# Optimization experiments

Hardware: AMD Instinct MI355X
Metric: run time of the kernel (lower is better)

## Reference

```python
import jax, jax.numpy as jnp
import numpy as np


def setup_inputs() -> dict:
    key = jax.random.key(0)
    k1, k2, k3 = jax.random.split(key, 3)
    B, T, F, U = 32, 4096, 512, 512
    x = jax.random.normal(k1, (B, T, F), dtype=jnp.float32)
    W = jax.random.normal(k2, (F, U), dtype=jnp.float32)
    b = jnp.zeros((U,), dtype=jnp.float32)
    V = jax.random.uniform(k3, (U, 1), dtype=jnp.float32)
    return {"x": x, "W": W, "b": b, "V": V}


def reference(x, W, b, V):
    # u = tanh(x @ W + b): [B, T, U]
    u = jnp.tanh(jnp.einsum('btf,fu->btu', x, W) + b)
    # scores = u @ V: [B, T, 1]; softmax over time (dim=1)
    a = jax.nn.softmax(jnp.einsum('btu,uo->bto', u, V), axis=1)
    # weighted sum pooling over time -> [B, F]
    return jnp.sum(x * a, axis=1)
```

## Files before the change

### kernel.cpp

```cpp
#include <hip/hip_runtime.h>


#define XT 4096
#define XF 512
#define XU 512

typedef __attribute__((ext_vector_type(8))) short short8;
typedef __attribute__((ext_vector_type(4))) short sh4;
typedef __attribute__((ext_vector_type(16))) float f32x16;

__device__ inline void cvt_hilo(float x, unsigned short &h, unsigned short &l) {
  unsigned u = __builtin_bit_cast(unsigned, x);
  h = (unsigned short)(u >> 16);
  float hf = __builtin_bit_cast(float, u & 0xFFFF0000u);
  float lo = x - hf;
  l = (unsigned short)(__builtin_bit_cast(unsigned, lo) >> 16);
}

__device__ inline float tanh_fast(float z) {
  float e = __expf(2.0f * z);
  return 1.0f - 2.0f * __builtin_amdgcn_rcpf(e + 1.0f);
}

__global__ void wconv_kernel(const float *__restrict__ W,
                             unsigned short *__restrict__ whi,
                             unsigned short *__restrict__ wlo) {
  int t2 = blockIdx.x * 256 + threadIdx.x;
  int l = t2 & 31;
  int g = (t2 >> 5) & 1;
  int t = (t2 >> 6) & 15;
  int s = t2 >> 10;
  short8 hv, lv;
#pragma unroll
  for (int j = 0; j < 8; ++j) {
    unsigned short h, lo;
    cvt_hilo(W[(size_t)(s * 16 + g * 8 + j) * XU + t * 32 + l], h, lo);
    hv[j] = (short)h;
    lv[j] = (short)lo;
  }
  size_t off = (size_t)s * 8192 + t * 512 + g * 256 + l * 8;
  *(short8 *)(whi + off) = hv;
  *(short8 *)(wlo + off) = lv;
}

#define MFMA(a, b, c) __builtin_amdgcn_mfma_f32_32x32x16_bf16(a, b, c, 0, 0, 0)

__global__ __launch_bounds__(512, 4)
void gemm_scores_kernel(const float *__restrict__ x,
                        const unsigned short *__restrict__ whi,
                        const unsigned short *__restrict__ wlo,
                        const float *__restrict__ bias,
                        const float *__restrict__ V,
                        float *__restrict__ partial,
                        float *__restrict__ pstats) {
  __shared__ unsigned short Abuf[2][4096];
  __shared__ float scb[256];
  __shared__ float sarr[128];
  __shared__ float warr[128];
  __shared__ float red[1536];

  const int tid = threadIdx.x;
  const int lane = tid & 63;
  const int w = tid >> 6;
  const int l31 = lane & 31;
  const int half = lane >> 5;
  const size_t rowbase = (size_t)blockIdx.x * 128;

  const int srow = tid >> 4;
  const int q = tid & 15;
  const int widx = (q >> 2) * 1024 + ((q >> 1) & 1) * 256 + srow * 8 + (q & 1) * 4;

  auto stage = [&](unsigned short *ab, float4 v) {
    sh4 h, l;
    unsigned short hh, ll;
    cvt_hilo(v.x, hh, ll); h[0] = (short)hh; l[0] = (short)ll;
    cvt_hilo(v.y, hh, ll); h[1] = (short)hh; l[1] = (short)ll;
    cvt_hilo(v.z, hh, ll); h[2] = (short)hh; l[2] = (short)ll;
    cvt_hilo(v.w, hh, ll); h[3] = (short)hh; l[3] = (short)ll;
    *(sh4 *)(ab + widx) = h;
    *(sh4 *)(ab + widx + 512) = l;
  };

  const unsigned short *whp = whi + (size_t)(w * 2) * 512 + lane * 8;
  const unsigned short *wlp = wlo + (size_t)(w * 2) * 512 + lane * 8;

#pragma unroll 1
  for (int sub = 0; sub < 4; ++sub) {
    f32x16 acc[2];
#pragma unroll
    for (int c = 0; c < 2; ++c)
#pragma unroll
      for (int r = 0; r < 16; ++r) acc[c][r] = 0.f;

    const float *sx = x + (rowbase + sub * 32 + srow) * XF + q * 4;

    float4 xa = *(const float4 *)sx;
    stage(&Abuf[0][0], xa);
    __syncthreads();

#pragma unroll 1
    for (int it = 0; it < 8; ++it) {
      float4 xn;
      if (it < 7) xn = *(const float4 *)(sx + (it + 1) * 64);

      const unsigned short *abase = &Abuf[it & 1][0];
      const unsigned short *pw = whp + (size_t)it * 32768;
      const unsigned short *pl = wlp + (size_t)it * 32768;

#pragma unroll 2
      for (int s16 = 0; s16 < 4; ++s16) {
        short8 bh0 = *(const short8 *)(pw + s16 * 8192);
        short8 bh1 = *(const short8 *)(pw + s16 * 8192 + 512);
        short8 bl0 = *(const short8 *)(pl + s16 * 8192);
        short8 bl1 = *(const short8 *)(pl + s16 * 8192 + 512);
        short8 ah = *(const short8 *)(abase + s16 * 1024 + lane * 8);
        short8 al = *(const short8 *)(abase + s16 * 1024 + 512 + lane * 8);
        acc[0] = MFMA(ah, bh0, acc[0]);
        acc[1] = MFMA(ah, bh1, acc[1]);
        acc[0] = MFMA(al, bh0, acc[0]);
        acc[1] = MFMA(al, bh1, acc[1]);
        acc[0] = MFMA(ah, bl0, acc[0]);
        acc[1] = MFMA(ah, bl1, acc[1]);
      }

      if (it < 7) stage(&Abuf[(it + 1) & 1][0], xn);
      __syncthreads();
    }

    float sc[16];
#pragma unroll
    for (int r = 0; r < 16; ++r) sc[r] = 0.f;
#pragma unroll
    for (int cf = 0; cf < 2; ++cf) {
      int n = w * 64 + cf * 32 + l31;
      float vv = V[n];
      float bb = bias[n];
#pragma unroll
      for (int r = 0; r < 16; ++r)
        sc[r] += tanh_fast(acc[cf][r] + bb) * vv;
    }
#pragma unroll
    for (int m = 1; m <= 16; m <<= 1) {
#pragma unroll
      for (int r = 0; r < 16; ++r) sc[r] += __shfl_xor(sc[r], m, 64);
    }
    if (l31 == 0) {
#pragma unroll
      for (int r = 0; r < 16; ++r) {
        int row = (r & 3) + 8 * (r >> 2) + 4 * half;
        scb[w * 32 + row] = sc[r];
      }
    }
    __syncthreads();
    if (tid < 32) {
      float s = 0.f;
#pragma unroll
      for (int ww = 0; ww < 8; ++ww) s += scb[ww * 32 + tid];
      sarr[sub * 32 + tid] = s;
    }
    __syncthreads();
  }

  float mloc = -1e30f;
#pragma unroll 8
  for (int i = 0; i < 128; ++i) mloc = fmaxf(mloc, sarr[i]);
  if (tid < 128) warr[tid] = __expf(sarr[tid] - mloc);
  __syncthreads();

  float lsum = 0.f;
  if (tid < 64) {
    lsum = warr[tid] + warr[tid + 64];
#pragma unroll
    for (int m = 1; m < 64; m <<= 1) lsum += __shfl_xor(lsum, m, 64);
  }

  const int rg = tid >> 7;
  const int c4 = tid & 127;
  const float *xp = x + rowbase * XF;
  float4 pa = {0.f, 0.f, 0.f, 0.f};
#pragma unroll 8
  for (int i = 0; i < 32; ++i) {
    int r = rg * 32 + i;
    float4 v = *(const float4 *)(xp + (size_t)r * XF + c4 * 4);
    float wv = warr[r];
    pa.x += wv * v.x;
    pa.y += wv * v.y;
    pa.z += wv * v.z;
    pa.w += wv * v.w;
  }
  if (rg > 0) {
    float *rp = red + (rg - 1) * 512 + c4 * 4;
    rp[0] = pa.x; rp[1] = pa.y; rp[2] = pa.z; rp[3] = pa.w;
  }
  __syncthreads();
  if (rg == 0) {
    const float *r0 = red + c4 * 4;
    float4 o;
    o.x = pa.x + r0[0] + r0[512] + r0[1024];
    o.y = pa.y + r0[1] + r0[513] + r0[1025];
    o.z = pa.z + r0[2] + r0[514] + r0[1026];
    o.w = pa.w + r0[3] + r0[515] + r0[1027];
    *(float4 *)(partial + (size_t)blockIdx.x * 512 + c4 * 4) = o;
  }
  if (tid == 0) {
    pstats[blockIdx.x * 2] = mloc;
    pstats[blockIdx.x * 2 + 1] = lsum;
  }
}

__global__ __launch_bounds__(512)
void combine_kernel(const float *__restrict__ partial,
                    const float *__restrict__ pstats,
                    float *__restrict__ out) {
  int b = blockIdx.x;
  int f = threadIdx.x;
  __shared__ float ml[32], ll[32];
  if (f < 32) {
    ml[f] = pstats[(b * 32 + f) * 2];
    ll[f] = pstats[(b * 32 + f) * 2 + 1];
  }
  __syncthreads();
  float M = -1e30f;
#pragma unroll
  for (int c = 0; c < 32; ++c) M = fmaxf(M, ml[c]);
  float L = 0.f;
#pragma unroll
  for (int c = 0; c < 32; ++c) L += __expf(ml[c] - M) * ll[c];
  float acc = 0.f;
#pragma unroll
  for (int c = 0; c < 32; ++c)
    acc += __expf(ml[c] - M) * partial[(size_t)(b * 32 + c) * 512 + f];
  out[b * XF + f] = acc / L;
}

extern "C" void kernel_launch(void *const *d_in, const int *in_sizes, int n_in,
                              void *d_out, int out_size, void *d_ws,
                              size_t ws_size, hipStream_t stream) {
  const float *x = (const float *)d_in[0];
  const float *W = (const float *)d_in[1];
  const float *bias = (const float *)d_in[2];
  const float *V = (const float *)d_in[3];
  float *out = (float *)d_out;

  unsigned short *whi = (unsigned short *)d_ws;
  unsigned short *wlo = whi + 262144;
  float *partial = (float *)((char *)d_ws + 1048576);
  float *pstats = (float *)((char *)d_ws + 1048576 + 2097152);

  wconv_kernel<<<128, 256, 0, stream>>>(W, whi, wlo);
  gemm_scores_kernel<<<1024, 512, 0, stream>>>(x, whi, wlo, bias, V, partial,
                                               pstats);
  combine_kernel<<<32, 512, 0, stream>>>(partial, pstats, out);
}
```

Measured before the change: 565.6 us.

## Stage W tiles in shared memory and keep 128x256 accumulators per wave group

The GEMM loop is restructured. Each block now keeps all 128 rows resident across 8 waves, arranged as 4 row slices by 2 column halves with 8 accumulator tiles each. The split-bf16 W tiles are double-buffered through shared memory and the x fragments are converted straight from registers, instead of staging x in LDS and streaming W from global per wave. The goal is more MFMA work per loaded byte, better W reuse and fewer barriers. The cost is 128 KB of shared memory and higher register pressure, which forces the occupancy hint down from 4 to 2 blocks per CU.

```diff
diff --git a/kernel.cpp b/kernel.cpp
--- a/kernel.cpp
+++ b/kernel.cpp
@@ -6,7 +6,6 @@
 #define XU 512
 
 typedef __attribute__((ext_vector_type(8))) short short8;
-typedef __attribute__((ext_vector_type(4))) short sh4;
 typedef __attribute__((ext_vector_type(16))) float f32x16;
 
 __device__ inline void cvt_hilo(float x, unsigned short &h, unsigned short &l) {
@@ -45,7 +44,7 @@
 
 #define MFMA(a, b, c) __builtin_amdgcn_mfma_f32_32x32x16_bf16(a, b, c, 0, 0, 0)
 
-__global__ __launch_bounds__(512, 4)
+__global__ __launch_bounds__(512, 2)
 void gemm_scores_kernel(const float *__restrict__ x,
                         const unsigned short *__restrict__ whi,
                         const unsigned short *__restrict__ wlo,
@@ -53,7 +52,7 @@
                         const float *__restrict__ V,
                         float *__restrict__ partial,
                         float *__restrict__ pstats) {
-  __shared__ unsigned short Abuf[2][4096];
+  __shared__ unsigned short Bsh[2][4][8192];
   __shared__ float scb[256];
   __shared__ float sarr[128];
   __shared__ float warr[128];
@@ -61,106 +60,135 @@
 
   const int tid = threadIdx.x;
   const int lane = tid & 63;
-  const int w = tid >> 6;
+  const int wave = tid >> 6;
+  const int rs = wave & 3;
+  const int c = wave >> 2;
   const int l31 = lane & 31;
   const int half = lane >> 5;
   const size_t rowbase = (size_t)blockIdx.x * 128;
 
-  const int srow = tid >> 4;
-  const int q = tid & 15;
-  const int widx = (q >> 2) * 1024 + ((q >> 1) & 1) * 256 + srow * 8 + (q & 1) * 4;
-
-  auto stage = [&](unsigned short *ab, float4 v) {
-    sh4 h, l;
-    unsigned short hh, ll;
-    cvt_hilo(v.x, hh, ll); h[0] = (short)hh; l[0] = (short)ll;
-    cvt_hilo(v.y, hh, ll); h[1] = (short)hh; l[1] = (short)ll;
-    cvt_hilo(v.z, hh, ll); h[2] = (short)hh; l[2] = (short)ll;
-    cvt_hilo(v.w, hh, ll); h[3] = (short)hh; l[3] = (short)ll;
-    *(sh4 *)(ab + widx) = h;
-    *(sh4 *)(ab + widx + 512) = l;
-  };
-
-  const unsigned short *whp = whi + (size_t)(w * 2) * 512 + lane * 8;
-  const unsigned short *wlp = wlo + (size_t)(w * 2) * 512 + lane * 8;
+  f32x16 acc[8];
+#pragma unroll
+  for (int cf = 0; cf < 8; ++cf)
+#pragma unroll
+    for (int r = 0; r < 16; ++r) acc[cf][r] = 0.f;
+
+  const float *xr = x + (rowbase + rs * 32 + l31) * XF + half * 8;
+  const int toff = tid * 8;
+  const int fbase = (c * 8) * 512 + lane * 8;
+
+  short8 st0, st1, st2, st3, st4, st5, st6, st7;
+  float4 xa0, xa1, xa2, xa3;
+
+#define LOADSTG(J)                                                   \
+  {                                                                  \
+    const unsigned short *ph = whi + (size_t)(2 * (J)) * 8192;       \
+    const unsigned short *pl = wlo + (size_t)(2 * (J)) * 8192;       \
+    st0 = *(const short8 *)(ph + toff);                              \
+    st1 = *(const short8 *)(ph + 4096 + toff);                       \
+    st2 = *(const short8 *)(pl + toff);                              \
+    st3 = *(const short8 *)(pl + 4096 + toff);                       \
+    st4 = *(const short8 *)(ph + 8192 + toff);                       \
+    st5 = *(const short8 *)(ph + 12288 + toff);                      \
+    st6 = *(const short8 *)(pl + 8192 + toff);                       \
+    st7 = *(const short8 *)(pl + 12288 + toff);                      \
+  }
+#define WRITESTG(BUF)                                                \
+  {                                                                  \
+    unsigned short *d = &Bsh[BUF][0][0] + toff;                      \
+    *(short8 *)(d) = st0;                                            \
+    *(short8 *)(d + 4096) = st1;                                     \
+    *(short8 *)(d + 8192) = st2;                                     \
+    *(short8 *)(d + 12288) = st3;                                    \
+    *(short8 *)(d + 16384) = st4;                                    \
+    *(short8 *)(d + 20480) = st5;                                    \
+    *(short8 *)(d + 24576) = st6;                                    \
+    *(short8 *)(d + 28672) = st7;                                    \
+  }
+#define LOADA(J)                                                     \
+  {                                                                  \
+    xa0 = *(const float4 *)(xr + (J) * 32);                          \
+    xa1 = *(const float4 *)(xr + (J) * 32 + 4);                      \
+    xa2 = *(const float4 *)(xr + (J) * 32 + 16);                     \
+    xa3 = *(const float4 *)(xr + (J) * 32 + 20);                     \
+  }
+
+  LOADSTG(0);
+  LOADA(0);
+  WRITESTG(0);
+  __syncthreads();
 
 #pragma unroll 1
-  for (int sub = 0; sub < 4; ++sub) {
-    f32x16 acc[2];
-#pragma unroll
-    for (int c = 0; c < 2; ++c)
-#pragma unroll
-      for (int r = 0; r < 16; ++r) acc[c][r] = 0.f;
-
-    const float *sx = x + (rowbase + sub * 32 + srow) * XF + q * 4;
-
-    float4 xa = *(const float4 *)sx;
-    stage(&Abuf[0][0], xa);
+  for (int j = 0; j < 16; ++j) {
+    const int cur = j & 1;
+
+    short8 ah0, al0, ah1, al1;
+    {
+      float v0[8] = {xa0.x, xa0.y, xa0.z, xa0.w, xa1.x, xa1.y, xa1.z, xa1.w};
+      float v1[8] = {xa2.x, xa2.y, xa2.z, xa2.w, xa3.x, xa3.y, xa3.z, xa3.w};
+#pragma unroll
+      for (int jj = 0; jj < 8; ++jj) {
+        unsigned short h, lo;
+        cvt_hilo(v0[jj], h, lo);
+        ah0[jj] = (short)h; al0[jj] = (short)lo;
+        cvt_hilo(v1[jj], h, lo);
+        ah1[jj] = (short)h; al1[jj] = (short)lo;
+      }
+    }
+
+    if (j < 15) {
+      LOADSTG(j + 1);
+      LOADA(j + 1);
+    }
+
+#pragma unroll
+    for (int h = 0; h < 2; ++h) {
+      const unsigned short *bp = &Bsh[cur][h * 2][0] + fbase;
+      const unsigned short *lp = bp + 8192;
+      short8 ahf = h ? ah1 : ah0;
+      short8 alf = h ? al1 : al0;
+#pragma unroll
+      for (int cf = 0; cf < 8; ++cf) {
+        short8 bh = *(const short8 *)(bp + cf * 512);
+        short8 bl = *(const short8 *)(lp + cf * 512);
+        acc[cf] = MFMA(ahf, bh, acc[cf]);
+        acc[cf] = MFMA(alf, bh, acc[cf]);
+        acc[cf] = MFMA(ahf, bl, acc[cf]);
+      }
+    }
+
+    if (j < 15) WRITESTG(cur ^ 1);
     __syncthreads();
-
-#pragma unroll 1
-    for (int it = 0; it < 8; ++it) {
-      float4 xn;
-      if (it < 7) xn = *(const float4 *)(sx + (it + 1) * 64);
-
-      const unsigned short *abase = &Abuf[it & 1][0];
-      const unsigned short *pw = whp + (size_t)it * 32768;
-      const unsigned short *pl = wlp + (size_t)it * 32768;
-
-#pragma unroll 2
-      for (int s16 = 0; s16 < 4; ++s16) {
-        short8 bh0 = *(const short8 *)(pw + s16 * 8192);
-        short8 bh1 = *(const short8 *)(pw + s16 * 8192 + 512);
-        short8 bl0 = *(const short8 *)(pl + s16 * 8192);
-        short8 bl1 = *(const short8 *)(pl + s16 * 8192 + 512);
-        short8 ah = *(const short8 *)(abase + s16 * 1024 + lane * 8);
-        short8 al = *(const short8 *)(abase + s16 * 1024 + 512 + lane * 8);
-        acc[0] = MFMA(ah, bh0, acc[0]);
-        acc[1] = MFMA(ah, bh1, acc[1]);
-        acc[0] = MFMA(al, bh0, acc[0]);
-        acc[1] = MFMA(al, bh1, acc[1]);
-        acc[0] = MFMA(ah, bl0, acc[0]);
-        acc[1] = MFMA(ah, bl1, acc[1]);
-      }
-
-      if (it < 7) stage(&Abuf[(it + 1) & 1][0], xn);
-      __syncthreads();
-    }
-
-    float sc[16];
-#pragma unroll
-    for (int r = 0; r < 16; ++r) sc[r] = 0.f;
-#pragma unroll
-    for (int cf = 0; cf < 2; ++cf) {
-      int n = w * 64 + cf * 32 + l31;
-      float vv = V[n];
-      float bb = bias[n];
-#pragma unroll
-      for (int r = 0; r < 16; ++r)
-        sc[r] += tanh_fast(acc[cf][r] + bb) * vv;
-    }
-#pragma unroll
-    for (int m = 1; m <= 16; m <<= 1) {
-#pragma unroll
-      for (int r = 0; r < 16; ++r) sc[r] += __shfl_xor(sc[r], m, 64);
-    }
-    if (l31 == 0) {
-#pragma unroll
-      for (int r = 0; r < 16; ++r) {
-        int row = (r & 3) + 8 * (r >> 2) + 4 * half;
-        scb[w * 32 + row] = sc[r];
-      }
-    }
-    __syncthreads();
-    if (tid < 32) {
-      float s = 0.f;
-#pragma unroll
-      for (int ww = 0; ww < 8; ++ww) s += scb[ww * 32 + tid];
-      sarr[sub * 32 + tid] = s;
-    }
-    __syncthreads();
-  }
-
+  }
+
+  float sc[16];
+#pragma unroll
+  for (int r = 0; r < 16; ++r) sc[r] = 0.f;
+#pragma unroll
+  for (int cf = 0; cf < 8; ++cf) {
+    int n = c * 256 + cf * 32 + l31;
+    float vv = V[n];
+    float bb = bias[n];
+#pragma unroll
+    for (int r = 0; r < 16; ++r)
+      sc[r] += tanh_fast(acc[cf][r] + bb) * vv;
+  }
+#pragma unroll
+  for (int m = 1; m <= 16; m <<= 1) {
+#pragma unroll
+    for (int r = 0; r < 16; ++r) sc[r] += __shfl_xor(sc[r], m, 64);
+  }
+  if (l31 == 0) {
+#pragma unroll
+    for (int r = 0; r < 16; ++r) {
+      int row = rs * 32 + (r & 3) + 8 * (r >> 2) + 4 * half;
+      scb[c * 128 + row] = sc[r];
+    }
+  }
+  __syncthreads();
+
+  if (tid < 128) sarr[tid] = scb[tid] + scb[128 + tid];
+  __syncthreads();
   float mloc = -1e30f;
 #pragma unroll 8
   for (int i = 0; i < 128; ++i) mloc = fmaxf(mloc, sarr[i]);
```

New measurement: 527.7 us. 6.7% less time.
